# Optimization experiments

Hardware: AMD Instinct MI355X
Metric: run time of the kernel (lower is better)

## Reference

```python
import jax, jax.numpy as jnp
import numpy as np

N = 4  # hypercomplex dimension

def setup_inputs() -> dict:
    key = jax.random.key(0)
    k1, k2, k3 = jax.random.split(key, 3)
    x = jax.random.normal(k1, (32, 196, 768), dtype=jnp.float32)
    # [n, out_pad/n, in_pad/n] = [4, 3072//4, 768//4]
    weight_components = jax.random.normal(k2, (N, 768, 192), dtype=jnp.float32) * 0.02
    bias = jax.random.normal(k3, (3072,), dtype=jnp.float32) * 0.02
    return {"x": x, "weight_components": weight_components, "bias": bias}

def reference(x, weight_components, bias):
    n, out_blk, in_blk = weight_components.shape
    batch_shape = x.shape[:-1]
    xb = x.reshape(-1, n, in_blk)  # [B, n, in_blk]
    # original: out[:, (i+j)%n] += x[:, j] @ W[i].T
    # equivalently out[:, k] = sum_j x[:, j] @ W[(k-j)%n].T
    k_idx = jnp.arange(n)[:, None]
    j_idx = jnp.arange(n)[None, :]
    Wperm = weight_components[(k_idx - j_idx) % n]  # [n(k), n(j), out_blk, in_blk]
    out = jnp.einsum('bjc,kjoc->bko', xb, Wperm)    # [B, n, out_blk]
    out = out.reshape(-1, n * out_blk) + bias
    return out.reshape(*batch_shape, n * out_blk)
```

## Files before the change

kernel.cpp:

```cpp
#include <hip/hip_runtime.h>
#include <stdint.h>

#define M_ROWS 6272
#define K_DIM  768
#define N_DIM  3072
#define BM 128
#define BN 256
#define BK 32
#define NITER (K_DIM / BK)

#define X_CHUNKS (M_ROWS * K_DIM / 8)
#define W_CHUNKS (N_DIM * K_DIM / 8)
#define X_BLOCKS (X_CHUNKS / 256)
#define W_BLOCKS (W_CHUNKS / 256)

#define GRID_X (N_DIM / BN)
#define GRID_Y (M_ROWS / BM)
#define NWG    (GRID_X * GRID_Y)

typedef unsigned short u16;
typedef __attribute__((ext_vector_type(8))) __bf16 bf16x8;
typedef __attribute__((ext_vector_type(4))) float f32x4;

__device__ __forceinline__ u16 f32_to_bf16(float f) {
    unsigned u = __float_as_uint(f);
    unsigned r = 0x7FFFu + ((u >> 16) & 1u);
    return (u16)((u + r) >> 16);
}

__device__ __forceinline__ unsigned pack2(float a, float b) {
    return (unsigned)f32_to_bf16(a) | ((unsigned)f32_to_bf16(b) << 16);
}

#define GLOAD16(gp, lp) __builtin_amdgcn_global_load_lds( \
    (const __attribute__((address_space(1))) void*)(gp),  \
    (__attribute__((address_space(3))) void*)(lp), 16, 0, 0)

__global__ void prep_kernel(const float* __restrict__ x, const float* __restrict__ w,
                            u16* __restrict__ xb, u16* __restrict__ wb) {
    int b = blockIdx.x;
    if (b < X_BLOCKS) {
        int idx = b * 256 + threadIdx.x;
        const float4* xp = (const float4*)x + (size_t)idx * 2;
        float4 a = xp[0], c = xp[1];
        uint4 v;
        v.x = pack2(a.x, a.y);
        v.y = pack2(a.z, a.w);
        v.z = pack2(c.x, c.y);
        v.w = pack2(c.z, c.w);
        ((uint4*)xb)[idx] = v;
    } else {
        int idx = (b - X_BLOCKS) * 256 + threadIdx.x;
        int n    = idx / 96;
        int kc   = idx - n * 96;
        int kblk = n / 768;
        int o    = n - kblk * 768;
        int j    = kc / 24;
        int c8   = kc - j * 24;
        int i    = (kblk - j) & 3;
        const float* src = w + (((size_t)i * 768 + o) * 192 + c8 * 8);
        float4 a = ((const float4*)src)[0];
        float4 c = ((const float4*)src)[1];
        uint4 v;
        v.x = pack2(a.x, a.y);
        v.y = pack2(a.z, a.w);
        v.z = pack2(c.x, c.y);
        v.w = pack2(c.z, c.w);
        ((uint4*)wb)[idx] = v;
    }
}

__global__ __launch_bounds__(256, 2) void gemm_bt(
    const u16* __restrict__ A,
    const u16* __restrict__ B,
    const float* __restrict__ bias,
    float* __restrict__ C)
{
    __shared__ __align__(16) u16 As[3][BM * BK];
    __shared__ __align__(16) u16 Bs[3][BN * BK];

    const int orig = blockIdx.x;
    const int xcd  = orig & 7;
    const int pos  = orig >> 3;
    const int q    = NWG >> 3;
    const int r    = NWG & 7;
    const int lin  = (xcd < r ? xcd * (q + 1) : r * (q + 1) + (xcd - r) * q) + pos;
    const int rowBlk = lin / GRID_X;
    const int colBlk = lin - rowBlk * GRID_X;

    const int rowBase = rowBlk * BM;
    const int colBase = colBlk * BN;

    const int tid    = threadIdx.x;
    const int wave   = tid >> 6;
    const int lane   = tid & 63;
    const int lane16 = lane & 15;
    const int quad   = lane >> 4;
    const int wc     = wave;

    const int rA = tid >> 2;
    const int sA = (tid & 3) ^ ((rA >> 1) & 3);

    const uint4* Ag = (const uint4*)(A + (size_t)(rowBase + rA) * K_DIM + sA * 8);
    const uint4* Bg = (const uint4*)(B + (size_t)(colBase + rA) * K_DIM + sA * 8);
    const int rowStride = 64 * (K_DIM / 8);

    char* AsB = (char*)As + wave * 1024;
    char* BsB = (char*)Bs + wave * 1024;

#define ISSUE(g, b) do {                                                    \
        GLOAD16(Ag + (g) * 4,                 AsB + (b) * 8192);            \
        GLOAD16(Ag + (g) * 4 + rowStride,     AsB + (b) * 8192 + 4096);     \
        GLOAD16(Bg + (g) * 4,                 BsB + (b) * 16384);           \
        GLOAD16(Bg + (g) * 4 + rowStride,     BsB + (b) * 16384 + 4096);    \
        GLOAD16(Bg + (g) * 4 + 2 * rowStride, BsB + (b) * 16384 + 8192);    \
        GLOAD16(Bg + (g) * 4 + 3 * rowStride, BsB + (b) * 16384 + 12288);   \
    } while (0)

    const int swz  = (lane16 >> 1) & 3;
    const int slot = (quad ^ swz) * 8;
    int aoff[8], boff[4];
#pragma unroll
    for (int i = 0; i < 8; ++i)
        aoff[i] = (i * 16 + lane16) * BK + slot;
#pragma unroll
    for (int j = 0; j < 4; ++j)
        boff[j] = (wc * 64 + j * 16 + lane16) * BK + slot;

    f32x4 acc[8][4] = {};

#define DS_READS(cb)                                                        \
    _Pragma("unroll") for (int i = 0; i < 8; ++i)                           \
        af[i] = *(const bf16x8*)&As[cb][aoff[i]];                           \
    _Pragma("unroll") for (int j = 0; j < 4; ++j)                           \
        bfv[j] = *(const bf16x8*)&Bs[cb][boff[j]];

#define MFMA32()                                                            \
    __builtin_amdgcn_s_setprio(1);                                          \
    _Pragma("unroll") for (int i = 0; i < 8; ++i)                           \
    _Pragma("unroll") for (int j = 0; j < 4; ++j)                           \
        acc[i][j] = __builtin_amdgcn_mfma_f32_16x16x32_bf16(                \
            af[i], bfv[j], acc[i][j], 0, 0, 0);                             \
    __builtin_amdgcn_s_setprio(0);

#define ITER_ISSUE(cb, fb, g) {                                             \
        bf16x8 af[8], bfv[4];                                               \
        DS_READS(cb)                                                        \
        ISSUE(g, fb);                                                       \
        asm volatile("s_waitcnt vmcnt(6)" ::: "memory");                    \
        asm volatile("s_waitcnt lgkmcnt(0)\n\ts_barrier" ::: "memory");     \
        MFMA32()                                                            \
    }

#define ITER_DRAIN(cb) {                                                    \
        bf16x8 af[8], bfv[4];                                               \
        DS_READS(cb)                                                        \
        asm volatile("s_waitcnt vmcnt(0)" ::: "memory");                    \
        asm volatile("s_waitcnt lgkmcnt(0)\n\ts_barrier" ::: "memory");     \
        MFMA32()                                                            \
    }

#define ITER_FINAL(cb) {                                                    \
        bf16x8 af[8], bfv[4];                                               \
        DS_READS(cb)                                                        \
        MFMA32()                                                            \
    }

    ISSUE(0, 0);
    ISSUE(1, 1);
    asm volatile("s_waitcnt vmcnt(6)\n\ts_barrier" ::: "memory");

    for (int t = 0; t < 7; ++t) {
        const int g = t * 3;
        ITER_ISSUE(0, 2, g + 2);
        ITER_ISSUE(1, 0, g + 3);
        ITER_ISSUE(2, 1, g + 4);
    }
    ITER_ISSUE(0, 2, 23);
    ITER_DRAIN(1);
    ITER_FINAL(2);

    float bv[4];
#pragma unroll
    for (int j = 0; j < 4; ++j)
        bv[j] = bias[colBase + wc * 64 + j * 16 + lane16];
#pragma unroll
    for (int i = 0; i < 8; ++i) {
        int row0 = rowBase + i * 16 + quad * 4;
#pragma unroll
        for (int r2 = 0; r2 < 4; ++r2) {
            float* cp = C + (size_t)(row0 + r2) * N_DIM + colBase + wc * 64 + lane16;
#pragma unroll
            for (int j = 0; j < 4; ++j)
                cp[j * 16] = acc[i][j][r2] + bv[j];
        }
    }
#undef ISSUE
#undef DS_READS
#undef MFMA32
#undef ITER_ISSUE
#undef ITER_DRAIN
#undef ITER_FINAL
}

extern "C" void kernel_launch(void* const* d_in, const int* in_sizes, int n_in,
                              void* d_out, int out_size, void* d_ws, size_t ws_size,
                              hipStream_t stream) {
    const float* x    = (const float*)d_in[0];
    const float* w    = (const float*)d_in[1];
    const float* bias = (const float*)d_in[2];
    float* out = (float*)d_out;

    u16* xb = (u16*)d_ws;
    u16* wb = (u16*)((char*)d_ws + (size_t)M_ROWS * K_DIM * 2);

    hipLaunchKernelGGL(prep_kernel, dim3(X_BLOCKS + W_BLOCKS), dim3(256),
                       0, stream, x, w, xb, wb);
    hipLaunchKernelGGL(gemm_bt, dim3(NWG), dim3(256),
                       0, stream, xb, wb, bias, out);
}
```

Before: 136.1 us.

## Switch GEMM to double-buffered LDS with three blocks per CU

Reduces the LDS pipeline from three stages to two, shrinking shared memory per block. The launch bound is raised so three workgroups can reside per CU. The main loop now issues the next tile's loads first, computes on the current tile, then waits for all loads and barriers. This trades prefetch depth and latency hiding within a block for more resident waves, and risks register pressure under the tighter bound.

```diff
diff --git a/kernel.cpp b/kernel.cpp
--- a/kernel.cpp
+++ b/kernel.cpp
@@ -70,14 +70,14 @@
     }
 }
 
-__global__ __launch_bounds__(256, 2) void gemm_bt(
+__global__ __launch_bounds__(256, 3) void gemm_bt(
     const u16* __restrict__ A,
     const u16* __restrict__ B,
     const float* __restrict__ bias,
     float* __restrict__ C)
 {
-    __shared__ __align__(16) u16 As[3][BM * BK];
-    __shared__ __align__(16) u16 Bs[3][BN * BK];
+    __shared__ __align__(16) u16 As[2][BM * BK];
+    __shared__ __align__(16) u16 Bs[2][BN * BK];
 
     const int orig = blockIdx.x;
     const int xcd  = orig & 7;
@@ -143,42 +143,29 @@
             af[i], bfv[j], acc[i][j], 0, 0, 0);                             \
     __builtin_amdgcn_s_setprio(0);
 
-#define ITER_ISSUE(cb, fb, g) {                                             \
+#define ITER(cur, nxt, g) {                                                 \
+        ISSUE(g, nxt);                                                      \
         bf16x8 af[8], bfv[4];                                               \
-        DS_READS(cb)                                                        \
-        ISSUE(g, fb);                                                       \
-        asm volatile("s_waitcnt vmcnt(6)" ::: "memory");                    \
-        asm volatile("s_waitcnt lgkmcnt(0)\n\ts_barrier" ::: "memory");     \
+        DS_READS(cur)                                                       \
         MFMA32()                                                            \
-    }
-
-#define ITER_DRAIN(cb) {                                                    \
+        asm volatile("s_waitcnt vmcnt(0) lgkmcnt(0)\n\ts_barrier" ::: "memory"); \
+    }
+
+#define ITER_FINAL(cur) {                                                   \
         bf16x8 af[8], bfv[4];                                               \
-        DS_READS(cb)                                                        \
-        asm volatile("s_waitcnt vmcnt(0)" ::: "memory");                    \
-        asm volatile("s_waitcnt lgkmcnt(0)\n\ts_barrier" ::: "memory");     \
+        DS_READS(cur)                                                       \
         MFMA32()                                                            \
     }
 
-#define ITER_FINAL(cb) {                                                    \
-        bf16x8 af[8], bfv[4];                                               \
-        DS_READS(cb)                                                        \
-        MFMA32()                                                            \
-    }
-
     ISSUE(0, 0);
-    ISSUE(1, 1);
-    asm volatile("s_waitcnt vmcnt(6)\n\ts_barrier" ::: "memory");
-
-    for (int t = 0; t < 7; ++t) {
-        const int g = t * 3;
-        ITER_ISSUE(0, 2, g + 2);
-        ITER_ISSUE(1, 0, g + 3);
-        ITER_ISSUE(2, 1, g + 4);
-    }
-    ITER_ISSUE(0, 2, 23);
-    ITER_DRAIN(1);
-    ITER_FINAL(2);
+    asm volatile("s_waitcnt vmcnt(0)\n\ts_barrier" ::: "memory");
+
+    for (int t = 0; t < 22; t += 2) {
+        ITER(0, 1, t + 1);
+        ITER(1, 0, t + 2);
+    }
+    ITER(0, 1, 23);
+    ITER_FINAL(1);
 
     float bv[4];
 #pragma unroll
@@ -198,8 +185,7 @@
 #undef ISSUE
 #undef DS_READS
 #undef MFMA32
-#undef ITER_ISSUE
-#undef ITER_DRAIN
+#undef ITER
 #undef ITER_FINAL
 }
 
```

Result: slower. 228.1 us (+67.6%).
